# Kernel tuning notes

Hardware: AMD Instinct MI355X
Metric: run time of the kernel (lower is better)

Reference implementation:

```python
import jax, jax.numpy as jnp
import numpy as np

HID = 1024     # hidden_dim
HEADS = 8      # num_heads
HD = HID // HEADS  # head_dim = 128
MD = 8         # manifold_dim
L = 3          # num_layers
B, S = 8, 1024
EPS = 1e-7
BALL_MAX = 1.0 - 1e-5  # clamp inside Poincare ball (|curvature| = 1)


def expmap0(v):
    """Hyperbolic exponential map at origin, curvature -1 (Poincare ball)."""
    n = jnp.sqrt(jnp.sum(v * v, axis=-1, keepdims=True))
    n = jnp.maximum(n, EPS)
    return jnp.tanh(n) * v / n


def logmap0(y):
    """Hyperbolic logarithm map at origin, curvature -1 (Poincare ball)."""
    n = jnp.sqrt(jnp.sum(y * y, axis=-1, keepdims=True))
    n_c = jnp.clip(n, EPS, BALL_MAX)
    return jnp.arctanh(n_c) * y / n_c


def setup_inputs() -> dict:
    key = jax.random.key(0)
    ks = jax.random.split(key, 6)
    sc = 0.02
    return {
        "x": jax.random.normal(ks[0], (B, S, HID), dtype=jnp.float32),
        "W_qkv": jax.random.normal(ks[1], (HID, 3 * HID), dtype=jnp.float32) * sc,
        "b_qkv": jnp.zeros((3 * HID,), dtype=jnp.float32),
        "W_pinv": jax.random.normal(ks[2], (HID, MD), dtype=jnp.float32) * sc,
        "b_pinv": jnp.zeros((MD,), dtype=jnp.float32),
        "W_attn": jax.random.normal(ks[3], (L, MD, HID), dtype=jnp.float32) * sc,
        "b_attn": jnp.zeros((L, HID), dtype=jnp.float32),
        "W_out": jax.random.normal(ks[4], (HID, HID), dtype=jnp.float32) * sc,
        "b_out": jnp.zeros((HID,), dtype=jnp.float32),
    }


def reference(x, W_qkv, b_qkv, W_pinv, b_pinv, W_attn, b_attn, W_out, b_out):
    inv_sqrt_d = 1.0 / np.sqrt(HD).astype(np.float32)
    cur = x
    for l in range(L):
        qkv = jnp.einsum('bsh,hd->bsd', cur, W_qkv) + b_qkv  # [B,S,3*HID]
        q, k, v = jnp.split(qkv, 3, axis=-1)
        # [B,S,HID] -> [B,HEADS,S,HD]
        def heads(t):
            return t.reshape(B, S, HEADS, HD).transpose(0, 2, 1, 3)
        q, k, v = heads(q), heads(k), heads(v)
        # geometric 'flow': hyperbolic retraction of Q/K onto the Poincare ball
        # (parallel transport at the origin is identity)
        qf = expmap0(q)
        kf = expmap0(k)
        scores = jnp.einsum('bhqd,bhkd->bhqk', qf, kf) * inv_sqrt_d
        att = jax.nn.softmax(scores, axis=-1)
        o = jnp.einsum('bhqk,bhkd->bhqd', att, v)  # [B,H,S,HD]
        o = o.transpose(0, 2, 1, 3).reshape(B, S, HID)
        # project to manifold coords, then per-layer pattern projection back
        m = jnp.einsum('bsh,hm->bsm', o, W_pinv) + b_pinv           # [B,S,MD]
        upd = jnp.einsum('bsm,mh->bsh', m, W_attn[l]) + b_attn[l]   # [B,S,HID]
        cur = cur + upd
    return jnp.einsum('bsh,hd->bsd', cur, W_out) + b_out
```

## Files before the change

kernel.cpp:

```cpp
#include <hip/hip_runtime.h>
#include <hip/hip_bf16.h>
#include <hip/hip_fp8.h>
#include <cstdint>

typedef __hip_bfloat16 bf16;
typedef __bf16 b8 __attribute__((ext_vector_type(8)));
typedef float f4v __attribute__((ext_vector_type(4)));
typedef short s8v __attribute__((ext_vector_type(8)));
typedef int i8v __attribute__((ext_vector_type(8)));

#define DEVI static __device__ __forceinline__

DEVI void gload16(const void* g, void* l) {
  __builtin_amdgcn_global_load_lds(
      (const __attribute__((address_space(1))) void*)(uintptr_t)g,
      (__attribute__((address_space(3))) void*)(uint32_t)(uintptr_t)l,
      16, 0, 0);
}

DEVI f4v mfma_bf16(b8 a, b8 b, f4v c) {
  return __builtin_amdgcn_mfma_f32_16x16x32_bf16(a, b, c, 0, 0, 0);
}

DEVI f4v mfma_fp8(i8v a, i8v b, f4v c) {
  return __builtin_amdgcn_mfma_scale_f32_16x16x128_f8f6f4(
      a, b, c, 0, 0, 0, 0x7F7F7F7F, 0, 0x7F7F7F7F);
}

DEVI uint8_t to_fp8(float f) {
  __hip_fp8_e4m3 v(f);
  return v.__x;
}

__global__ void prep_kernel(const float* __restrict__ x, float* __restrict__ cur,
                            bf16* __restrict__ curb, uint8_t* __restrict__ curf8) {
  int i = (blockIdx.x * 256 + threadIdx.x) * 4;
  float4 v = *(const float4*)(x + i);
  *(float4*)(cur + i) = v;
  __hip_bfloat162 a, b;
  a.x = __float2bfloat16(v.x); a.y = __float2bfloat16(v.y);
  b.x = __float2bfloat16(v.z); b.y = __float2bfloat16(v.w);
  *(__hip_bfloat162*)(curb + i) = a;
  *(__hip_bfloat162*)(curb + i + 2) = b;
  uint32_t p = (uint32_t)to_fp8(v.x) | ((uint32_t)to_fp8(v.y) << 8) |
               ((uint32_t)to_fp8(v.z) << 16) | ((uint32_t)to_fp8(v.w) << 24);
  *(uint32_t*)(curf8 + i) = p;
}

__global__ void transpose_cast(const float* __restrict__ in, bf16* __restrict__ out,
                               int R, int C) {
  __shared__ float tile[32][33];
  int c0 = blockIdx.x * 32, r0 = blockIdx.y * 32;
  int tx = threadIdx.x & 31, ty = threadIdx.x >> 5;
  for (int rr = ty; rr < 32; rr += 8)
    tile[rr][tx] = in[(size_t)(r0 + rr) * C + c0 + tx];
  __syncthreads();
  for (int cc = ty; cc < 32; cc += 8)
    out[(size_t)(c0 + cc) * R + r0 + tx] = __float2bfloat16(tile[tx][cc]);
}

__global__ void transpose_cast_fp8(const float* __restrict__ in,
                                   uint8_t* __restrict__ out, int R, int C) {
  __shared__ float tile[32][33];
  int c0 = blockIdx.x * 32, r0 = blockIdx.y * 32;
  int tx = threadIdx.x & 31, ty = threadIdx.x >> 5;
  for (int rr = ty; rr < 32; rr += 8)
    tile[rr][tx] = in[(size_t)(r0 + rr) * C + c0 + tx];
  __syncthreads();
  for (int cc = ty; cc < 32; cc += 8)
    out[(size_t)(c0 + cc) * R + r0 + tx] = to_fp8(tile[tx][cc]);
}

__global__ __launch_bounds__(256, 3)
void gemm_qkv_fp8(const uint8_t* __restrict__ A, const uint8_t* __restrict__ Bt,
                  const float* __restrict__ bias, bf16* __restrict__ Qo,
                  bf16* __restrict__ Ko, bf16* __restrict__ Vto, int M, int N,
                  int K) {
  __shared__ uint8_t As[128 * 128];
  __shared__ uint8_t Bs[128 * 128];
  __shared__ float red[2][128];
  const int t = threadIdx.x;
  const int w = t >> 6, lane = t & 63;
  const int lm = lane & 15, qd = lane >> 4;
  const int m0 = blockIdx.x * 128, n0 = blockIdx.y * 128;
  const int wm = (w & 1) * 64, wn = (w >> 1) * 64;

  const uint8_t* Ag = A + (size_t)m0 * K;
  const uint8_t* Bg = Bt + (size_t)n0 * K;

  f4v acc[4][4];
  f4v zero = {0.f, 0.f, 0.f, 0.f};
#pragma unroll
  for (int i = 0; i < 4; i++)
#pragma unroll
    for (int j = 0; j < 4; j++) acc[i][j] = zero;

  for (int k0 = 0; k0 < K; k0 += 128) {
#pragma unroll
    for (int c = 0; c < 4; c++) {
      int s = c * 256 + t;
      int r = s >> 3;
      int kc = (s & 7) ^ (r & 7);
      gload16(Ag + (size_t)r * K + k0 + kc * 16, &As[s * 16]);
      gload16(Bg + (size_t)r * K + k0 + kc * 16, &Bs[s * 16]);
    }
    __syncthreads();
    i8v af[4], bfr[4];
#pragma unroll
    for (int tm = 0; tm < 4; tm++) {
      int row = wm + tm * 16 + lm;
      int ch = (qd * 2) ^ (row & 7);
      union { int4 q[2]; i8v v; } u;
      u.q[0] = *(const int4*)&As[row * 128 + ch * 16];
      u.q[1] = *(const int4*)&As[row * 128 + (ch ^ 1) * 16];
      af[tm] = u.v;
    }
#pragma unroll
    for (int tn = 0; tn < 4; tn++) {
      int row = wn + tn * 16 + lm;
      int ch = (qd * 2) ^ (row & 7);
      union { int4 q[2]; i8v v; } u;
      u.q[0] = *(const int4*)&Bs[row * 128 + ch * 16];
      u.q[1] = *(const int4*)&Bs[row * 128 + (ch ^ 1) * 16];
      bfr[tn] = u.v;
    }
#pragma unroll
    for (int tm = 0; tm < 4; tm++)
#pragma unroll
      for (int tn = 0; tn < 4; tn++)
        acc[tm][tn] = mfma_fp8(af[tm], bfr[tn], acc[tm][tn]);
    __syncthreads();
  }

  const int part = n0 >> 10;
  const int hh = (n0 >> 7) & 7;
  if (part == 2) {
#pragma unroll
    for (int tm = 0; tm < 4; tm++)
#pragma unroll
      for (int tn = 0; tn < 4; tn++) {
        int d = wn + tn * 16 + lm;
        float bv = bias[n0 + d];
        int row0 = m0 + wm + tm * 16 + qd * 4;
        int b = row0 >> 10, s0 = row0 & 1023;
        bf16 vt[4];
#pragma unroll
        for (int r = 0; r < 4; r++) vt[r] = __float2bfloat16(acc[tm][tn][r] + bv);
        *(ushort4*)&Vto[((size_t)(b * 8 + hh)) * 131072 + (size_t)d * 1024 + s0] =
            *(ushort4*)vt;
      }
  } else {
    float bvs[4];
#pragma unroll
    for (int tn = 0; tn < 4; tn++) bvs[tn] = bias[n0 + wn + tn * 16 + lm];
    float ss[4][4];
#pragma unroll
    for (int tm = 0; tm < 4; tm++)
#pragma unroll
      for (int r = 0; r < 4; r++) {
        float s = 0.f;
#pragma unroll
        for (int tn = 0; tn < 4; tn++) {
          float v = acc[tm][tn][r] + bvs[tn];
          s += v * v;
        }
#pragma unroll
        for (int off = 1; off < 16; off <<= 1) s += __shfl_xor(s, off, 64);
        ss[tm][r] = s;
      }
    if (lm == 0) {
#pragma unroll
      for (int tm = 0; tm < 4; tm++)
#pragma unroll
        for (int r = 0; r < 4; r++)
          red[w >> 1][wm + tm * 16 + qd * 4 + r] = ss[tm][r];
    }
    __syncthreads();
    const float qsc = (part == 0) ? 0.08838834764831845f : 1.0f;
    float scr[4][4];
#pragma unroll
    for (int tm = 0; tm < 4; tm++)
#pragma unroll
      for (int r = 0; r < 4; r++) {
        int row = wm + tm * 16 + qd * 4 + r;
        float tot = red[0][row] + red[1][row];
        float nrm = fmaxf(sqrtf(tot), 1e-7f);
        scr[tm][r] = tanhf(nrm) / nrm * qsc;
      }
    bf16* dst = (part == 0) ? Qo : Ko;
#pragma unroll
    for (int tm = 0; tm < 4; tm++)
#pragma unroll
      for (int tn = 0; tn < 4; tn++) {
        int d = wn + tn * 16 + lm;
        int row0 = m0 + wm + tm * 16 + qd * 4;
        int b = row0 >> 10, s0 = row0 & 1023;
#pragma unroll
        for (int r = 0; r < 4; r++)
          dst[(((size_t)(b * 8 + hh)) * 1024 + s0 + r) * 128 + d] =
              __float2bfloat16((acc[tm][tn][r] + bvs[tn]) * scr[tm][r]);
      }
  }
}

__global__ __launch_bounds__(256, 3)
void gemm_bt(const bf16* __restrict__ A, const bf16* __restrict__ Bt,
             const float* __restrict__ bias, float* __restrict__ Cf, int M, int N,
             int K) {
  __shared__ bf16 As[128 * 64];
  __shared__ bf16 Bs[128 * 64];
  const int t = threadIdx.x;
  const int w = t >> 6, lane = t & 63;
  const int lm = lane & 15, qd = lane >> 4;
  const int m0 = blockIdx.x * 128, n0 = blockIdx.y * 128;
  const int wm = (w & 1) * 64, wn = (w >> 1) * 64;

  const bf16* Ag = A + (size_t)m0 * K;
  const bf16* Bg = Bt + (size_t)n0 * K;

  f4v acc[4][4];
  f4v zero = {0.f, 0.f, 0.f, 0.f};
#pragma unroll
  for (int i = 0; i < 4; i++)
#pragma unroll
    for (int j = 0; j < 4; j++) acc[i][j] = zero;

  for (int k0 = 0; k0 < K; k0 += 64) {
#pragma unroll
    for (int c = 0; c < 4; c++) {
      int s = c * 256 + t;
      int r = s >> 3;
      int kc = (s & 7) ^ (r & 7);
      gload16(Ag + (size_t)r * K + k0 + kc * 8, &As[s * 8]);
      gload16(Bg + (size_t)r * K + k0 + kc * 8, &Bs[s * 8]);
    }
    __syncthreads();
#pragma unroll
    for (int ks = 0; ks < 2; ks++) {
      b8 af[4], bfr[4];
#pragma unroll
      for (int tm = 0; tm < 4; tm++) {
        int row = wm + tm * 16 + lm;
        int ch = (ks * 4 + qd) ^ (row & 7);
        af[tm] = *(const b8*)&As[row * 64 + ch * 8];
      }
#pragma unroll
      for (int tn = 0; tn < 4; tn++) {
        int row = wn + tn * 16 + lm;
        int ch = (ks * 4 + qd) ^ (row & 7);
        bfr[tn] = *(const b8*)&Bs[row * 64 + ch * 8];
      }
#pragma unroll
      for (int tm = 0; tm < 4; tm++)
#pragma unroll
        for (int tn = 0; tn < 4; tn++)
          acc[tm][tn] = mfma_bf16(af[tm], bfr[tn], acc[tm][tn]);
    }
    __syncthreads();
  }

#pragma unroll
  for (int tm = 0; tm < 4; tm++)
#pragma unroll
    for (int tn = 0; tn < 4; tn++) {
      int col = n0 + wn + tn * 16 + lm;
      float bv = bias[col];
#pragma unroll
      for (int r = 0; r < 4; r++) {
        int row = m0 + wm + tm * 16 + qd * 4 + r;
        Cf[(size_t)row * N + col] = acc[tm][tn][r] + bv;
      }
    }
}

__global__ __launch_bounds__(256, 2)
void attn_kernel(const bf16* __restrict__ Qf, const bf16* __restrict__ Kf,
                 const bf16* __restrict__ Vt, bf16* __restrict__ O) {
  __shared__ bf16 smem[40960];
  bf16* Ps = smem + 32768;
  const int t = threadIdx.x, w = t >> 6, lane = t & 63;
  const int lm = lane & 15, qd = lane >> 4;
  const int bh = blockIdx.x, qt = blockIdx.y;
  const bf16* Qg = Qf + ((size_t)bh * 1024 + qt * 128) * 128;
  const bf16* Kg = Kf + (size_t)bh * 131072;
  const bf16* Vg = Vt + (size_t)bh * 131072;
  bf16* Pw = Ps + w * 2048;

  auto stage = [&](int kt, int b) {
    bf16* Ksb = smem + b * 16384;
    bf16* Vsb = Ksb + 8192;
#pragma unroll
    for (int c = 0; c < 4; c++) {
      int s = c * 256 + t;
      int r = s >> 4;
      int kc = (s & 15) ^ (r & 7);
      gload16(Kg + (size_t)(kt * 64 + r) * 128 + kc * 8, &Ksb[s * 8]);
      int rv = s >> 3;
      int kv = (s & 7) ^ (rv & 7);
      gload16(Vg + (size_t)rv * 1024 + kt * 64 + kv * 8, &Vsb[s * 8]);
    }
  };

  b8 qfr[2][4];
#pragma unroll
  for (int mt = 0; mt < 2; mt++)
#pragma unroll
    for (int ks = 0; ks < 4; ks++)
      qfr[mt][ks] =
          *(const b8*)(Qg + (size_t)(w * 32 + mt * 16 + lm) * 128 + ks * 32 + qd * 8);

  f4v o[2][8];
  f4v lacc[2];
  f4v zero = {0.f, 0.f, 0.f, 0.f};
#pragma unroll
  for (int mt = 0; mt < 2; mt++) {
    lacc[mt] = zero;
#pragma unroll
    for (int i = 0; i < 8; i++) o[mt][i] = zero;
  }
  union { s8v s; b8 b; } uo;
#pragma unroll
  for (int i = 0; i < 8; i++) uo.s[i] = 0x3F80;
  const b8 ones = uo.b;

  stage(0, 0);
  for (int kt = 0; kt < 16; kt++) {
    const int cb = kt & 1;
    if (kt < 15) {
      stage(kt + 1, cb ^ 1);
      asm volatile("s_waitcnt vmcnt(8)" ::: "memory");
    } else {
      asm volatile("s_waitcnt vmcnt(0)" ::: "memory");
    }
    __builtin_amdgcn_sched_barrier(0);
    __builtin_amdgcn_s_barrier();
    __builtin_amdgcn_sched_barrier(0);
    const bf16* Ks = smem + cb * 16384;
    const bf16* Vs = Ks + 8192;

    f4v sc[2][4];
#pragma unroll
    for (int mt = 0; mt < 2; mt++)
#pragma unroll
      for (int tn = 0; tn < 4; tn++) sc[mt][tn] = zero;
    __builtin_amdgcn_s_setprio(1);
#pragma unroll
    for (int tn = 0; tn < 4; tn++) {
      int krow = tn * 16 + lm;
#pragma unroll
      for (int ks = 0; ks < 4; ks++) {
        int ch = (ks * 4 + qd) ^ (krow & 7);
        b8 kfr = *(const b8*)&Ks[krow * 128 + ch * 8];
        sc[0][tn] = mfma_bf16(qfr[0][ks], kfr, sc[0][tn]);
        sc[1][tn] = mfma_bf16(qfr[1][ks], kfr, sc[1][tn]);
      }
    }
    __builtin_amdgcn_s_setprio(0);
#pragma unroll
    for (int mt = 0; mt < 2; mt++)
#pragma unroll
      for (int tn = 0; tn < 4; tn++)
#pragma unroll
        for (int r = 0; r < 4; r++) {
          int qi = mt * 16 + qd * 4 + r;
          int ch = (tn * 2 + (lm >> 3)) ^ ((qi >> 1) & 7);
          Pw[qi * 64 + ch * 8 + (lm & 7)] = __float2bfloat16(__expf(sc[mt][tn][r]));
        }

    b8 pa[2][2];
#pragma unroll
    for (int mt = 0; mt < 2; mt++)
#pragma unroll
      for (int kv2 = 0; kv2 < 2; kv2++) {
        int qi = mt * 16 + lm;
        int ch = (kv2 * 4 + qd) ^ ((lm >> 1) & 7);
        pa[mt][kv2] = *(const b8*)&Pw[qi * 64 + ch * 8];
      }
    __builtin_amdgcn_s_setprio(1);
#pragma unroll
    for (int mt = 0; mt < 2; mt++)
#pragma unroll
      for (int kv2 = 0; kv2 < 2; kv2++)
        lacc[mt] = mfma_bf16(pa[mt][kv2], ones, lacc[mt]);
#pragma unroll
    for (int tnd = 0; tnd < 8; tnd++) {
      int drow = tnd * 16 + lm;
#pragma unroll
      for (int kv2 = 0; kv2 < 2; kv2++) {
        int ch = (kv2 * 4 + qd) ^ (drow & 7);
        b8 vfr = *(const b8*)&Vs[drow * 64 + ch * 8];
#pragma unroll
        for (int mt = 0; mt < 2; mt++)
          o[mt][tnd] = mfma_bf16(pa[mt][kv2], vfr, o[mt][tnd]);
      }
    }
    __builtin_amdgcn_s_setprio(0);
    __builtin_amdgcn_sched_barrier(0);
    __builtin_amdgcn_s_barrier();
  }

  const int b = bh >> 3, h = bh & 7;
#pragma unroll
  for (int mt = 0; mt < 2; mt++) {
    float rinv[4];
#pragma unroll
    for (int r = 0; r < 4; r++) rinv[r] = 1.0f / lacc[mt][r];
#pragma unroll
    for (int tnd = 0; tnd < 8; tnd++) {
      int d = tnd * 16 + lm;
#pragma unroll
      for (int r = 0; r < 4; r++) {
        int sIdx = qt * 128 + w * 32 + mt * 16 + qd * 4 + r;
        O[((size_t)b * 1024 + sIdx) * 1024 + h * 128 + d] =
            __float2bfloat16(o[mt][tnd][r] * rinv[r]);
      }
    }
  }
}

__global__ __launch_bounds__(256, 4)
void update_kernel(const bf16* __restrict__ O, const float* __restrict__ Wpinv,
                   const float* __restrict__ bpinv, const float* __restrict__ Wattn,
                   const float* __restrict__ battn, float* __restrict__ cur,
                   bf16* __restrict__ curb, uint8_t* __restrict__ curf8) {
  const int t = threadIdx.x, w = t >> 6, lane = t & 63;
  const int r0 = blockIdx.x * 8 + w * 2;
  const int hb = lane * 4;

  float a0[8], a1[8];
#pragma unroll
  for (int j = 0; j < 8; j++) { a0[j] = 0.f; a1[j] = 0.f; }
#pragma unroll
  for (int c = 0; c < 4; c++) {
    const bf16* p0 = O + (size_t)r0 * 1024 + c * 256 + hb;
    bf16 t0[4], t1[4];
    *(ushort4*)t0 = *(const ushort4*)p0;
    *(ushort4*)t1 = *(const ushort4*)(p0 + 1024);
#pragma unroll
    for (int e = 0; e < 4; e++) {
      float v0 = __bfloat162float(t0[e]);
      float v1 = __bfloat162float(t1[e]);
      const float* wr = Wpinv + (size_t)(c * 256 + hb + e) * 8;
      float4 wa = *(const float4*)wr;
      float4 wb = *(const float4*)(wr + 4);
      a0[0] += v0 * wa.x; a0[1] += v0 * wa.y;
      a0[2] += v0 * wa.z; a0[3] += v0 * wa.w;
      a0[4] += v0 * wb.x; a0[5] += v0 * wb.y;
      a0[6] += v0 * wb.z; a0[7] += v0 * wb.w;
      a1[0] += v1 * wa.x; a1[1] += v1 * wa.y;
      a1[2] += v1 * wa.z; a1[3] += v1 * wa.w;
      a1[4] += v1 * wb.x; a1[5] += v1 * wb.y;
      a1[6] += v1 * wb.z; a1[7] += v1 * wb.w;
    }
  }
#pragma unroll
  for (int j = 0; j < 8; j++) {
#pragma unroll
    for (int off = 32; off; off >>= 1) {
      a0[j] += __shfl_xor(a0[j], off, 64);
      a1[j] += __shfl_xor(a1[j], off, 64);
    }
  }
#pragma unroll
  for (int j = 0; j < 8; j++) {
    float bp = bpinv[j];
    a0[j] += bp;
    a1[j] += bp;
  }

#pragma unroll
  for (int c = 0; c < 4; c++) {
    float4 bv = *(const float4*)(battn + c * 256 + hb);
    float u00 = bv.x, u01 = bv.y, u02 = bv.z, u03 = bv.w;
    float u10 = bv.x, u11 = bv.y, u12 = bv.z, u13 = bv.w;
#pragma unroll
    for (int j = 0; j < 8; j++) {
      float4 wv = *(const float4*)(Wattn + (size_t)j * 1024 + c * 256 + hb);
      u00 += a0[j] * wv.x; u01 += a0[j] * wv.y;
      u02 += a0[j] * wv.z; u03 += a0[j] * wv.w;
      u10 += a1[j] * wv.x; u11 += a1[j] * wv.y;
      u12 += a1[j] * wv.z; u13 += a1[j] * wv.w;
    }
    {
      float* cp = cur + (size_t)r0 * 1024 + c * 256 + hb;
      float4 c4 = *(float4*)cp;
      c4.x += u00; c4.y += u01; c4.z += u02; c4.w += u03;
      *(float4*)cp = c4;
      bf16 cb[4];
      cb[0] = __float2bfloat16(c4.x); cb[1] = __float2bfloat16(c4.y);
      cb[2] = __float2bfloat16(c4.z); cb[3] = __float2bfloat16(c4.w);
      *(ushort4*)(curb + (size_t)r0 * 1024 + c * 256 + hb) = *(ushort4*)cb;
      uint32_t p = (uint32_t)to_fp8(c4.x) | ((uint32_t)to_fp8(c4.y) << 8) |
                   ((uint32_t)to_fp8(c4.z) << 16) | ((uint32_t)to_fp8(c4.w) << 24);
      *(uint32_t*)(curf8 + (size_t)r0 * 1024 + c * 256 + hb) = p;
    }
    {
      float* cp = cur + (size_t)(r0 + 1) * 1024 + c * 256 + hb;
      float4 c4 = *(float4*)cp;
      c4.x += u10; c4.y += u11; c4.z += u12; c4.w += u13;
      *(float4*)cp = c4;
      bf16 cb[4];
      cb[0] = __float2bfloat16(c4.x); cb[1] = __float2bfloat16(c4.y);
      cb[2] = __float2bfloat16(c4.z); cb[3] = __float2bfloat16(c4.w);
      *(ushort4*)(curb + (size_t)(r0 + 1) * 1024 + c * 256 + hb) = *(ushort4*)cb;
      uint32_t p = (uint32_t)to_fp8(c4.x) | ((uint32_t)to_fp8(c4.y) << 8) |
                   ((uint32_t)to_fp8(c4.z) << 16) | ((uint32_t)to_fp8(c4.w) << 24);
      *(uint32_t*)(curf8 + (size_t)(r0 + 1) * 1024 + c * 256 + hb) = p;
    }
  }
}

extern "C" void kernel_launch(void* const* d_in, const int* in_sizes, int n_in,
                              void* d_out, int out_size, void* d_ws, size_t ws_size,
                              hipStream_t stream) {
  const float* x      = (const float*)d_in[0];
  const float* W_qkv  = (const float*)d_in[1];
  const float* b_qkv  = (const float*)d_in[2];
  const float* W_pinv = (const float*)d_in[3];
  const float* b_pinv = (const float*)d_in[4];
  const float* W_attn = (const float*)d_in[5];
  const float* b_attn = (const float*)d_in[6];
  const float* W_out  = (const float*)d_in[7];
  const float* b_out  = (const float*)d_in[8];

  char* ws = (char*)d_ws;
  size_t off = 0;
  auto alloc = [&](size_t bytes) -> void* {
    void* p = ws + off;
    off += (bytes + 255) & ~(size_t)255;
    return p;
  };
  float* cur     = (float*)alloc((size_t)8192 * 1024 * 4);
  bf16* curb     = (bf16*)alloc((size_t)8192 * 1024 * 2);
  uint8_t* curf8 = (uint8_t*)alloc((size_t)8192 * 1024);
  uint8_t* Wqkv8 = (uint8_t*)alloc((size_t)3072 * 1024);
  bf16* Woutt    = (bf16*)alloc((size_t)1024 * 1024 * 2);
  bf16* Q        = (bf16*)alloc((size_t)8192 * 1024 * 2);
  bf16* Kt       = (bf16*)alloc((size_t)8192 * 1024 * 2);
  bf16* Vt       = (bf16*)alloc((size_t)8192 * 1024 * 2);
  bf16* O        = (bf16*)alloc((size_t)8192 * 1024 * 2);
  (void)ws_size; (void)in_sizes; (void)n_in; (void)out_size;

  prep_kernel<<<8192, 256, 0, stream>>>(x, cur, curb, curf8);
  transpose_cast_fp8<<<dim3(96, 32), 256, 0, stream>>>(W_qkv, Wqkv8, 1024, 3072);
  transpose_cast<<<dim3(32, 32), 256, 0, stream>>>(W_out, Woutt, 1024, 1024);

  for (int l = 0; l < 3; l++) {
    gemm_qkv_fp8<<<dim3(64, 24), 256, 0, stream>>>(curf8, Wqkv8, b_qkv, Q, Kt, Vt,
                                                   8192, 3072, 1024);
    attn_kernel<<<dim3(64, 8), 256, 0, stream>>>(Q, Kt, Vt, O);
    update_kernel<<<1024, 256, 0, stream>>>(O, W_pinv, b_pinv,
                                            W_attn + (size_t)l * 8 * 1024,
                                            b_attn + (size_t)l * 1024, cur, curb,
                                            curf8);
  }
  gemm_bt<<<dim3(64, 8), 256, 0, stream>>>(curb, Woutt, b_out, (float*)d_out, 8192,
                                           1024, 1024);
}
```

Baseline: 503.2 us.

## Fuse W_pinv projection into attention epilogue and add MFMA priority hints

```diff
diff --git a/kernel.cpp b/kernel.cpp
--- a/kernel.cpp
+++ b/kernel.cpp
@@ -124,11 +124,13 @@
       u.q[1] = *(const int4*)&Bs[row * 128 + (ch ^ 1) * 16];
       bfr[tn] = u.v;
     }
+    __builtin_amdgcn_s_setprio(1);
 #pragma unroll
     for (int tm = 0; tm < 4; tm++)
 #pragma unroll
       for (int tn = 0; tn < 4; tn++)
         acc[tm][tn] = mfma_fp8(af[tm], bfr[tn], acc[tm][tn]);
+    __builtin_amdgcn_s_setprio(0);
     __syncthreads();
   }
 
@@ -250,11 +252,13 @@
         int ch = (ks * 4 + qd) ^ (row & 7);
         bfr[tn] = *(const b8*)&Bs[row * 64 + ch * 8];
       }
+      __builtin_amdgcn_s_setprio(1);
 #pragma unroll
       for (int tm = 0; tm < 4; tm++)
 #pragma unroll
         for (int tn = 0; tn < 4; tn++)
           acc[tm][tn] = mfma_bf16(af[tm], bfr[tn], acc[tm][tn]);
+      __builtin_amdgcn_s_setprio(0);
     }
     __syncthreads();
   }
@@ -275,7 +279,8 @@
 
 __global__ __launch_bounds__(256, 2)
 void attn_kernel(const bf16* __restrict__ Qf, const bf16* __restrict__ Kf,
-                 const bf16* __restrict__ Vt, bf16* __restrict__ O) {
+                 const bf16* __restrict__ Vt, const float* __restrict__ Wpinv,
+                 float* __restrict__ Mpart) {
   __shared__ bf16 smem[40960];
   bf16* Ps = smem + 32768;
   const int t = threadIdx.x, w = t >> 6, lane = t & 63;
@@ -399,73 +404,75 @@
     __builtin_amdgcn_s_barrier();
   }
 
-  const int b = bh >> 3, h = bh & 7;
+  const int h = bh & 7;
+  float wp[8][8];
+#pragma unroll
+  for (int tnd = 0; tnd < 8; tnd++) {
+    const float* wr = Wpinv + (size_t)(h * 128 + tnd * 16 + lm) * 8;
+    float4 wa = *(const float4*)wr;
+    float4 wb = *(const float4*)(wr + 4);
+    wp[tnd][0] = wa.x; wp[tnd][1] = wa.y; wp[tnd][2] = wa.z; wp[tnd][3] = wa.w;
+    wp[tnd][4] = wb.x; wp[tnd][5] = wb.y; wp[tnd][6] = wb.z; wp[tnd][7] = wb.w;
+  }
 #pragma unroll
   for (int mt = 0; mt < 2; mt++) {
     float rinv[4];
 #pragma unroll
     for (int r = 0; r < 4; r++) rinv[r] = 1.0f / lacc[mt][r];
 #pragma unroll
-    for (int tnd = 0; tnd < 8; tnd++) {
-      int d = tnd * 16 + lm;
-#pragma unroll
-      for (int r = 0; r < 4; r++) {
+    for (int r = 0; r < 4; r++) {
+      float pm[8];
+#pragma unroll
+      for (int j = 0; j < 8; j++) pm[j] = 0.f;
+#pragma unroll
+      for (int tnd = 0; tnd < 8; tnd++) {
+        float ov = o[mt][tnd][r] * rinv[r];
+#pragma unroll
+        for (int j = 0; j < 8; j++) pm[j] += ov * wp[tnd][j];
+      }
+#pragma unroll
+      for (int j = 0; j < 8; j++) {
+#pragma unroll
+        for (int off = 1; off < 16; off <<= 1)
+          pm[j] += __shfl_xor(pm[j], off, 64);
+      }
+      float sv = pm[0];
+#pragma unroll
+      for (int j = 1; j < 8; j++) sv = (lm == j) ? pm[j] : sv;
+      if (lm < 8) {
         int sIdx = qt * 128 + w * 32 + mt * 16 + qd * 4 + r;
-        O[((size_t)b * 1024 + sIdx) * 1024 + h * 128 + d] =
-            __float2bfloat16(o[mt][tnd][r] * rinv[r]);
+        Mpart[((size_t)bh * 1024 + sIdx) * 8 + lm] = sv;
       }
     }
   }
 }
 
 __global__ __launch_bounds__(256, 4)
-void update_kernel(const bf16* __restrict__ O, const float* __restrict__ Wpinv,
-                   const float* __restrict__ bpinv, const float* __restrict__ Wattn,
-                   const float* __restrict__ battn, float* __restrict__ cur,
-                   bf16* __restrict__ curb, uint8_t* __restrict__ curf8) {
+void update_kernel(const float* __restrict__ Mpart, const float* __restrict__ bpinv,
+                   const float* __restrict__ Wattn, const float* __restrict__ battn,
+                   float* __restrict__ cur, bf16* __restrict__ curb,
+                   uint8_t* __restrict__ curf8) {
   const int t = threadIdx.x, w = t >> 6, lane = t & 63;
   const int r0 = blockIdx.x * 8 + w * 2;
   const int hb = lane * 4;
+  const int hh = lane >> 3, jj = lane & 7;
 
   float a0[8], a1[8];
-#pragma unroll
-  for (int j = 0; j < 8; j++) { a0[j] = 0.f; a1[j] = 0.f; }
-#pragma unroll
-  for (int c = 0; c < 4; c++) {
-    const bf16* p0 = O + (size_t)r0 * 1024 + c * 256 + hb;
-    bf16 t0[4], t1[4];
-    *(ushort4*)t0 = *(const ushort4*)p0;
-    *(ushort4*)t1 = *(const ushort4*)(p0 + 1024);
-#pragma unroll
-    for (int e = 0; e < 4; e++) {
-      float v0 = __bfloat162float(t0[e]);
-      float v1 = __bfloat162float(t1[e]);
-      const float* wr = Wpinv + (size_t)(c * 256 + hb + e) * 8;
-      float4 wa = *(const float4*)wr;
-      float4 wb = *(const float4*)(wr + 4);
-      a0[0] += v0 * wa.x; a0[1] += v0 * wa.y;
-      a0[2] += v0 * wa.z; a0[3] += v0 * wa.w;
-      a0[4] += v0 * wb.x; a0[5] += v0 * wb.y;
-      a0[6] += v0 * wb.z; a0[7] += v0 * wb.w;
-      a1[0] += v1 * wa.x; a1[1] += v1 * wa.y;
-      a1[2] += v1 * wa.z; a1[3] += v1 * wa.w;
-      a1[4] += v1 * wb.x; a1[5] += v1 * wb.y;
-      a1[6] += v1 * wb.z; a1[7] += v1 * wb.w;
-    }
-  }
-#pragma unroll
-  for (int j = 0; j < 8; j++) {
-#pragma unroll
-    for (int off = 32; off; off >>= 1) {
-      a0[j] += __shfl_xor(a0[j], off, 64);
-      a1[j] += __shfl_xor(a1[j], off, 64);
-    }
-  }
-#pragma unroll
-  for (int j = 0; j < 8; j++) {
-    float bp = bpinv[j];
-    a0[j] += bp;
-    a1[j] += bp;
+  {
+    const int b0 = r0 >> 10, s0 = r0 & 1023;
+    float v0 = Mpart[(((size_t)b0 * 8 + hh) * 1024 + s0) * 8 + jj];
+    float v1 = Mpart[(((size_t)b0 * 8 + hh) * 1024 + s0 + 1) * 8 + jj];
+#pragma unroll
+    for (int off = 8; off < 64; off <<= 1) {
+      v0 += __shfl_xor(v0, off, 64);
+      v1 += __shfl_xor(v1, off, 64);
+    }
+#pragma unroll
+    for (int j = 0; j < 8; j++) {
+      float bp = bpinv[j];
+      a0[j] = __shfl(v0, j, 64) + bp;
+      a1[j] = __shfl(v1, j, 64) + bp;
+    }
   }
 
 #pragma unroll
@@ -538,7 +545,7 @@
   bf16* Q        = (bf16*)alloc((size_t)8192 * 1024 * 2);
   bf16* Kt       = (bf16*)alloc((size_t)8192 * 1024 * 2);
   bf16* Vt       = (bf16*)alloc((size_t)8192 * 1024 * 2);
-  bf16* O        = (bf16*)alloc((size_t)8192 * 1024 * 2);
+  float* Mpart   = (float*)alloc((size_t)65536 * 8 * 4);
   (void)ws_size; (void)in_sizes; (void)n_in; (void)out_size;
 
   prep_kernel<<<8192, 256, 0, stream>>>(x, cur, curb, curf8);
@@ -548,8 +555,8 @@
   for (int l = 0; l < 3; l++) {
     gemm_qkv_fp8<<<dim3(64, 24), 256, 0, stream>>>(curf8, Wqkv8, b_qkv, Q, Kt, Vt,
                                                    8192, 3072, 1024);
-    attn_kernel<<<dim3(64, 8), 256, 0, stream>>>(Q, Kt, Vt, O);
-    update_kernel<<<1024, 256, 0, stream>>>(O, W_pinv, b_pinv,
+    attn_kernel<<<dim3(64, 8), 256, 0, stream>>>(Q, Kt, Vt, W_pinv, Mpart);
+    update_kernel<<<1024, 256, 0, stream>>>(Mpart, b_pinv,
                                             W_attn + (size_t)l * 8 * 1024,
                                             b_attn + (size_t)l * 1024, cur, curb,
                                             curf8);
```

New measurement: 450.7 us. 10.4% less time.
